# Kernel tuning notes

Measured on AMD Instinct MI355X. Metric: run time of the kernel, lower is better.

## Reference

```python
import jax, jax.numpy as jnp
import numpy as np

BETA = 0.25

def setup_inputs() -> dict:
    key = jax.random.key(0)
    kz, ke = jax.random.split(key)
    z = jax.random.normal(kz, (8, 256, 8, 32, 32), dtype=jnp.float32)
    num_codes, code_dim = 1024, 256
    # matches nn.init.uniform_(weight, -1/num_codes, 1/num_codes) in scale
    embed = jax.random.uniform(ke, (num_codes, code_dim), dtype=jnp.float32,
                               minval=-1.0 / num_codes, maxval=1.0 / num_codes)
    return {"z": z, "embed": embed}


def reference(z, embed):
    # z: (B, C, D, H, W); embed: (num_codes, code_dim) with C == code_dim
    B, C, D, H, W = z.shape
    num_codes = embed.shape[0]
    z_flat = jnp.transpose(z, (0, 2, 3, 4, 1)).reshape(-1, C)  # (N, C)

    # squared euclidean distances to all codes: ||z||^2 + ||e||^2 - 2 z.e
    dist = ((z_flat * z_flat).sum(axis=1, keepdims=True)
            + (embed * embed).sum(axis=1)
            - 2.0 * z_flat @ embed.T)  # (N, num_codes)
    indices = jnp.argmin(dist, axis=1)  # (N,) int
    z_q_flat = embed[indices]  # (N, C) gather

    # commitment loss (codebook is EMA-updated, so only beta * commitment)
    commitment = jnp.mean((z_flat - jax.lax.stop_gradient(z_q_flat)) ** 2)
    loss = BETA * commitment

    # straight-through estimator
    z_q_flat = z_flat + jax.lax.stop_gradient(z_q_flat - z_flat)
    z_q = jnp.transpose(z_q_flat.reshape(B, D, H, W, C), (0, 4, 1, 2, 3))

    # perplexity (scatter-add histogram instead of materializing one-hot)
    counts = jnp.zeros((num_codes,), dtype=z.dtype).at[indices].add(1.0)
    avg_probs = counts / indices.shape[0]
    perplexity = jnp.exp(-jnp.sum(avg_probs * jnp.log(avg_probs + 1e-10)))

    return z_q, indices.reshape(B, D, H, W), loss, perplexity
```

## Files before the change

kernel.cpp:

```cpp
#include <hip/hip_runtime.h>
#include <math.h>

#define Cdim   256
#define Ssp    8192
#define Npts   65536
#define NCODES 1024
#define BETA   0.25f
#define MT     64
#define NKC    48
#define ESCALE 8192.0f
#define WS_NEED (65536 + (size_t)786432 * 2)

typedef _Float16 f16;
typedef f16   half8  __attribute__((ext_vector_type(8)));
typedef float f32x16 __attribute__((ext_vector_type(16)));

#define MFMA16(A, B, C) __builtin_amdgcn_mfma_f32_32x32x16_f16(A, B, C, 0, 0, 0)

__global__ __launch_bounds__(256) void enorm_kernel(const float* __restrict__ embed,
                                                    float* __restrict__ enorm) {
    int j = blockIdx.x * 256 + threadIdx.x;
    if (j >= NCODES) return;
    const float4* row = reinterpret_cast<const float4*>(embed + (size_t)j * Cdim);
    float s = 0.f;
#pragma unroll 8
    for (int c4 = 0; c4 < Cdim / 4; ++c4) {
        float4 v = row[c4];
        s += v.x * v.x + v.y * v.y + v.z * v.z + v.w * v.w;
    }
    enorm[j] = s;
}

__global__ __launch_bounds__(256) void prep_kernel(const float* __restrict__ embed,
                                                   f16* __restrict__ Bws) {
    int tid = blockIdx.x * 256 + threadIdx.x;
    int o4 = tid * 4;
    int kc = o4 >> 14;
    int r  = o4 & 16383;
    int j  = r >> 4;
    int k0 = r & 15;
#pragma unroll
    for (int i = 0; i < 4; ++i) {
        int k = kc * 16 + k0 + i;
        int c = k & 255;
        float ev = embed[j * 256 + c] * ESCALE;
        f16 eh = (f16)ev;
        f16 v  = (k >= 256 && k < 512) ? (f16)(ev - (float)eh) : eh;
        Bws[o4 + i] = v;
    }
}

__global__ __launch_bounds__(256, 2) void vq_gemm(const float* __restrict__ z,
                                                  const f16* __restrict__ Bws,
                                                  const float* __restrict__ enorm,
                                                  float* __restrict__ out_idx,
                                                  float* __restrict__ counts) {
    __shared__ __attribute__((aligned(16))) f16 As[MT * 512];
    __shared__ float en_s[NCODES];
    __shared__ float znp[256];
    __shared__ float zn_s[MT];
    __shared__ float redv[8 * MT];
    __shared__ int   redi[8 * MT];

    const int t  = threadIdx.x;
    const int l  = t & 63;
    const int w  = t >> 6;
    const int ln = l & 31;
    const int kb = l >> 5;
    const int n0 = blockIdx.x * MT;
    const int b  = n0 >> 13;
    const int s0 = n0 & 8191;

    {
        const int p = t & 63;
        const int q = t >> 6;
        const float* zb = z + (size_t)b * ((size_t)Cdim * Ssp) + s0;
        float zsq = 0.f;
#pragma unroll
        for (int gi = 0; gi < 8; ++gi) {
            const int c0 = q * 64 + gi * 8;
            half8 hh, ll;
#pragma unroll
            for (int u = 0; u < 8; ++u) {
                float zv = zb[(size_t)(c0 + u) * Ssp + p];
                zsq += zv * zv;
                f16 zh = (f16)zv;
                hh[u] = zh;
                ll[u] = (f16)(zv - (float)zh);
            }
            const int g0 = c0 >> 3;
            *(half8*)&As[p * 512 + 8 * (g0 ^ (p & 7))]        = hh;
            *(half8*)&As[p * 512 + 8 * ((32 + g0) ^ (p & 7))] = ll;
        }
        znp[q * 64 + p] = zsq;
    }
    for (int i = t; i < NCODES; i += 256) en_s[i] = enorm[i];
    __syncthreads();
    if (t < MT) zn_s[t] = ((znp[t] + znp[64 + t]) + znp[128 + t]) + znp[192 + t];
    __syncthreads();

#pragma unroll 1
    for (int jh = 0; jh < 2; ++jh) {
        f32x16 acc[2][4] = {};
        const f16* bbase = Bws + (size_t)(jh * 512 + w * 128 + ln) * 16 + kb * 8;

        half8 b0 = *(const half8*)(bbase);
        half8 b1 = *(const half8*)(bbase + 512);
        half8 b2 = *(const half8*)(bbase + 1024);
        half8 b3 = *(const half8*)(bbase + 1536);

#pragma unroll 2
        for (int kc = 0; kc < NKC; ++kc) {
            const int gg = (kc < 16) ? (2 * kc + kb)
                         : (kc < 32) ? (2 * (kc - 16) + kb)
                                     : (32 + 2 * (kc - 32) + kb);
            const int gsw = 8 * (gg ^ (ln & 7));
            half8 a0 = *(const half8*)&As[ln * 512 + gsw];
            half8 a1 = *(const half8*)&As[(32 + ln) * 512 + gsw];

            half8 n0r = b0, n1 = b1, n2 = b2, n3 = b3;
            if (kc + 1 < NKC) {
                const f16* src = bbase + (size_t)(kc + 1) * 16384;
                n0r = *(const half8*)(src);
                n1  = *(const half8*)(src + 512);
                n2  = *(const half8*)(src + 1024);
                n3  = *(const half8*)(src + 1536);
            }
            acc[0][0] = MFMA16(a0, b0, acc[0][0]);
            acc[1][0] = MFMA16(a1, b0, acc[1][0]);
            acc[0][1] = MFMA16(a0, b1, acc[0][1]);
            acc[1][1] = MFMA16(a1, b1, acc[1][1]);
            acc[0][2] = MFMA16(a0, b2, acc[0][2]);
            acc[1][2] = MFMA16(a1, b2, acc[1][2]);
            acc[0][3] = MFMA16(a0, b3, acc[0][3]);
            acc[1][3] = MFMA16(a1, b3, acc[1][3]);
            b0 = n0r; b1 = n1; b2 = n2; b3 = n3;
        }

        const int h = l >> 5;
#pragma unroll
        for (int mm = 0; mm < 2; ++mm) {
#pragma unroll
            for (int rg = 0; rg < 16; ++rg) {
                const int row = mm * 32 + (rg & 3) + 8 * (rg >> 2) + 4 * h;
                const float znv = zn_s[row];
                float bv = 3.0e38f; int bi = 0;
#pragma unroll
                for (int nn = 0; nn < 4; ++nn) {
                    const int col = jh * 512 + w * 128 + nn * 32 + ln;
                    float k1 = znv + en_s[col];
                    float sc = k1 - acc[mm][nn][rg] * (2.0f / ESCALE);
                    if (sc < bv) { bv = sc; bi = col; }
                }
#pragma unroll
                for (int off = 1; off < 32; off <<= 1) {
                    float ov = __shfl_xor(bv, off, 64);
                    int   oi = __shfl_xor(bi, off, 64);
                    if (ov < bv || (ov == bv && oi < bi)) { bv = ov; bi = oi; }
                }
                if (ln == 0) {
                    redv[(jh * 4 + w) * MT + row] = bv;
                    redi[(jh * 4 + w) * MT + row] = bi;
                }
            }
        }
    }
    __syncthreads();
    if (t < MT) {
        float bv = redv[t]; int bi = redi[t];
#pragma unroll
        for (int s = 1; s < 8; ++s) {
            float ov = redv[s * MT + t]; int oi = redi[s * MT + t];
            if (ov < bv || (ov == bv && oi < bi)) { bv = ov; bi = oi; }
        }
        out_idx[n0 + t] = (float)bi;
        atomicAdd(&counts[bi], 1.0f);
    }
}

__global__ __launch_bounds__(256) void vq_epi(const float* __restrict__ z,
                                              const float* __restrict__ embed,
                                              const float* __restrict__ out_idx,
                                              float* __restrict__ out_zq,
                                              float* __restrict__ loss_acc) {
    const int n = blockIdx.x * 256 + threadIdx.x;
    const int b = n >> 13, s = n & 8191;
    const int idx = (int)out_idx[n];
    const float4* er = reinterpret_cast<const float4*>(embed + (size_t)idx * Cdim);
    const float* zp = z + (size_t)b * ((size_t)Cdim * Ssp) + s;
    float* oq = out_zq + (size_t)b * ((size_t)Cdim * Ssp) + s;
    float lsum = 0.f;
#pragma unroll 4
    for (int c4 = 0; c4 < Cdim / 4; ++c4) {
        float4 e = er[c4];
        const int c = c4 * 4;
        float z0 = zp[(size_t)(c + 0) * Ssp], z1 = zp[(size_t)(c + 1) * Ssp];
        float z2 = zp[(size_t)(c + 2) * Ssp], z3 = zp[(size_t)(c + 3) * Ssp];
        oq[(size_t)(c + 0) * Ssp] = e.x;
        oq[(size_t)(c + 1) * Ssp] = e.y;
        oq[(size_t)(c + 2) * Ssp] = e.z;
        oq[(size_t)(c + 3) * Ssp] = e.w;
        float d0 = z0 - e.x, d1 = z1 - e.y, d2 = z2 - e.z, d3 = z3 - e.w;
        lsum += d0 * d0 + d1 * d1 + d2 * d2 + d3 * d3;
    }
#pragma unroll
    for (int off = 32; off > 0; off >>= 1) lsum += __shfl_down(lsum, off, 64);
    if ((threadIdx.x & 63) == 0) atomicAdd(loss_acc, lsum);
}

#define PTS 64
#define CT  128
#define KC  32
__global__ __launch_bounds__(256, 2) void vq_main_fb(const float* __restrict__ z,
                                                     const float* __restrict__ embed,
                                                     const float* __restrict__ enorm,
                                                     float* __restrict__ out_zq,
                                                     float* __restrict__ out_idx,
                                                     float* __restrict__ loss_acc,
                                                     float* __restrict__ counts) {
    __shared__ __attribute__((aligned(16))) float smem[Cdim * PTS + KC * CT];
    float* zt = smem;
    float* et = smem + Cdim * PTS;
    const int t  = threadIdx.x;
    const int n0 = blockIdx.x * PTS;
    const int b  = n0 >> 13;
    const int s0 = n0 & 8191;
    const float* zb = z + (size_t)b * Cdim * Ssp + s0;
    {
        const int p4 = (t & 15) * 4, crow = t >> 4;
#pragma unroll
        for (int it = 0; it < 16; ++it) {
            int c = it * 16 + crow;
            float4 v = *reinterpret_cast<const float4*>(zb + (size_t)c * Ssp + p4);
            *reinterpret_cast<float4*>(&zt[c * PTS + p4]) = v;
        }
    }
    __syncthreads();
    {
        const int p = t & 63, qq = t >> 6;
        float sacc = 0.f;
#pragma unroll 8
        for (int c = qq * 64; c < qq * 64 + 64; ++c) { float v = zt[c * PTS + p]; sacc += v * v; }
        et[qq * 64 + p] = sacc;
    }
    __syncthreads();
    const int pg = t & 15, jg = t >> 4;
    const int p0 = pg * 4;
    float zn[4];
#pragma unroll
    for (int i = 0; i < 4; ++i) {
        int p = p0 + i;
        zn[i] = ((et[p] + et[64 + p]) + et[128 + p]) + et[192 + p];
    }
    float bestv[4] = {3.0e38f, 3.0e38f, 3.0e38f, 3.0e38f};
    int   besti[4] = {0, 0, 0, 0};
    const int dj = t >> 3, q = t & 7;
    const int sw_st = (q & 3) << 3;
    for (int jt = 0; jt < NCODES / CT; ++jt) {
        const int J0 = jt * CT;
        float acc[4][8];
#pragma unroll
        for (int i = 0; i < 4; ++i)
#pragma unroll
            for (int m = 0; m < 8; ++m) acc[i][m] = 0.f;
        for (int ks = 0; ks < Cdim / KC; ++ks) {
            const int cc0 = ks * KC;
            __syncthreads();
#pragma unroll
            for (int i = 0; i < 4; ++i) {
                const int jrel = dj + 32 * i;
                const float4 v = *reinterpret_cast<const float4*>(
                    embed + (size_t)(J0 + jrel) * Cdim + cc0 + q * 4);
                const int c0 = q * 4;
                const int jsw = jrel ^ sw_st;
                et[(c0 + 0) * CT + jsw] = v.x;
                et[(c0 + 1) * CT + jsw] = v.y;
                et[(c0 + 2) * CT + jsw] = v.z;
                et[(c0 + 3) * CT + jsw] = v.w;
            }
            __syncthreads();
#pragma unroll 4
            for (int c = 0; c < KC; ++c) {
                const float4 zp = *reinterpret_cast<const float4*>(&zt[(cc0 + c) * PTS + p0]);
                const int jb = (jg * 8) ^ (((c >> 2) & 3) << 3);
                const float4 ea = *reinterpret_cast<const float4*>(&et[c * CT + jb]);
                const float4 eb = *reinterpret_cast<const float4*>(&et[c * CT + jb + 4]);
                const float zc[4] = {zp.x, zp.y, zp.z, zp.w};
                const float ec[8] = {ea.x, ea.y, ea.z, ea.w, eb.x, eb.y, eb.z, eb.w};
#pragma unroll
                for (int i = 0; i < 4; ++i)
#pragma unroll
                    for (int m = 0; m < 8; ++m) acc[i][m] += zc[i] * ec[m];
            }
        }
#pragma unroll
        for (int m = 0; m < 8; ++m) {
            const int cid = J0 + jg * 8 + m;
            const float en = enorm[cid];
#pragma unroll
            for (int i = 0; i < 4; ++i) {
                float k1 = zn[i] + en;
                float sc = k1 - 2.0f * acc[i][m];
                if (sc < bestv[i]) { bestv[i] = sc; besti[i] = cid; }
            }
        }
    }
    __syncthreads();
    float* rv = et; int* ri = (int*)(et + 1024); int* idxf = (int*)(et + 2048);
#pragma unroll
    for (int i = 0; i < 4; ++i) { int p = p0 + i; rv[p * 16 + jg] = bestv[i]; ri[p * 16 + jg] = besti[i]; }
    __syncthreads();
    if (t < PTS) {
        int p = t;
        float bv = rv[p * 16]; int bi = ri[p * 16];
        for (int g = 1; g < 16; ++g) {
            float v = rv[p * 16 + g]; int ii = ri[p * 16 + g];
            if (v < bv || (v == bv && ii < bi)) { bv = v; bi = ii; }
        }
        idxf[p] = bi;
        out_idx[n0 + p] = (float)bi;
        atomicAdd(&counts[bi], 1.0f);
    }
    __syncthreads();
    float lsum = 0.f;
    {
        const int p = t & 63, cbase = t >> 6;
        const int myidx = idxf[p];
        const float4* erow4 = reinterpret_cast<const float4*>(embed + (size_t)myidx * Cdim);
        float* ob = out_zq + (size_t)b * Cdim * Ssp + s0 + p;
#pragma unroll 4
        for (int pass = 0; pass < 16; ++pass) {
            int c = cbase * 64 + pass * 4;
            float4 e = erow4[c >> 2];
            ob[(size_t)(c + 0) * Ssp] = e.x;
            ob[(size_t)(c + 1) * Ssp] = e.y;
            ob[(size_t)(c + 2) * Ssp] = e.z;
            ob[(size_t)(c + 3) * Ssp] = e.w;
            float d0 = zt[(c + 0) * PTS + p] - e.x;
            float d1 = zt[(c + 1) * PTS + p] - e.y;
            float d2 = zt[(c + 2) * PTS + p] - e.z;
            float d3 = zt[(c + 3) * PTS + p] - e.w;
            lsum += d0 * d0 + d1 * d1 + d2 * d2 + d3 * d3;
        }
    }
#pragma unroll
    for (int off = 32; off > 0; off >>= 1) lsum += __shfl_down(lsum, off, 64);
    if ((t & 63) == 0) atomicAdd(loss_acc, lsum);
}

__global__ __launch_bounds__(1024) void vq_final(const float* __restrict__ counts,
                                                 const float* __restrict__ loss_acc,
                                                 float* __restrict__ out_loss,
                                                 float* __restrict__ out_perp) {
    __shared__ float red[16];
    int t = threadIdx.x;
    float cnt = counts[t];
    float avg = cnt * (1.0f / (float)Npts);
    float term = avg * logf(avg + 1e-10f);
#pragma unroll
    for (int off = 32; off > 0; off >>= 1) term += __shfl_down(term, off, 64);
    if ((t & 63) == 0) red[t >> 6] = term;
    __syncthreads();
    if (t == 0) {
        float s = 0.f;
        for (int i = 0; i < 16; ++i) s += red[i];
        *out_perp = expf(-s);
        *out_loss = BETA * loss_acc[0] * (1.0f / 16777216.0f);
    }
}

extern "C" void kernel_launch(void* const* d_in, const int* in_sizes, int n_in,
                              void* d_out, int out_size, void* d_ws, size_t ws_size,
                              hipStream_t stream) {
    const float* z     = (const float*)d_in[0];
    const float* embed = (const float*)d_in[1];

    float* ws       = (float*)d_ws;
    float* loss_acc = ws;
    float* counts   = ws + 64;
    float* enorm    = ws + 2048;

    float* out_zq   = (float*)d_out;
    float* out_idx  = out_zq + (size_t)Npts * Cdim;
    float* out_loss = out_idx + Npts;
    float* out_perp = out_loss + 1;

    hipMemsetAsync(d_ws, 0, 2048 * sizeof(float), stream);
    enorm_kernel<<<NCODES / 256, 256, 0, stream>>>(embed, enorm);

    if (ws_size >= WS_NEED) {
        f16* Bws = (f16*)((char*)d_ws + 65536);
        prep_kernel<<<768, 256, 0, stream>>>(embed, Bws);
        vq_gemm<<<Npts / MT, 256, 0, stream>>>(z, Bws, enorm, out_idx, counts);
        vq_epi<<<Npts / 256, 256, 0, stream>>>(z, embed, out_idx, out_zq, loss_acc);
    } else {
        vq_main_fb<<<Npts / PTS, 256, 0, stream>>>(z, embed, enorm, out_zq, out_idx,
                                                   loss_acc, counts);
    }
    vq_final<<<1, 1024, 0, stream>>>(counts, loss_acc, out_loss, out_perp);
}
```

Before: 224.4 us.

## Fuse epilogue gather and loss into GEMM kernel, double-buffer B loads

Removes the separate epilogue kernel. The GEMM kernel now writes the gathered codebook rows to z_q directly with nontemporal stores. It computes the commitment loss from the winning distance value instead of re-reading z. The MFMA loop is restructured into a two-stage register double buffer for B fragments, and z reads use nontemporal loads. The fused path saves a full re-read of z and a launch. The risk is that the loss computed from the fp16-split distance may differ slightly in precision, and register pressure rises.

Measured after the change: 278.2 us. +24.0%, slower.

```diff
diff --git a/kernel.cpp b/kernel.cpp
--- a/kernel.cpp
+++ b/kernel.cpp
@@ -52,8 +52,11 @@
 
 __global__ __launch_bounds__(256, 2) void vq_gemm(const float* __restrict__ z,
                                                   const f16* __restrict__ Bws,
+                                                  const float* __restrict__ embed,
                                                   const float* __restrict__ enorm,
+                                                  float* __restrict__ out_zq,
                                                   float* __restrict__ out_idx,
+                                                  float* __restrict__ loss_acc,
                                                   float* __restrict__ counts) {
     __shared__ __attribute__((aligned(16))) f16 As[MT * 512];
     __shared__ float en_s[NCODES];
@@ -61,6 +64,7 @@
     __shared__ float zn_s[MT];
     __shared__ float redv[8 * MT];
     __shared__ int   redi[8 * MT];
+    __shared__ int   idxf[MT];
 
     const int t  = threadIdx.x;
     const int l  = t & 63;
@@ -82,7 +86,7 @@
             half8 hh, ll;
 #pragma unroll
             for (int u = 0; u < 8; ++u) {
-                float zv = zb[(size_t)(c0 + u) * Ssp + p];
+                float zv = __builtin_nontemporal_load(zb + (size_t)(c0 + u) * Ssp + p);
                 zsq += zv * zv;
                 f16 zh = (f16)zv;
                 hh[u] = zh;
@@ -104,37 +108,62 @@
         f32x16 acc[2][4] = {};
         const f16* bbase = Bws + (size_t)(jh * 512 + w * 128 + ln) * 16 + kb * 8;
 
-        half8 b0 = *(const half8*)(bbase);
-        half8 b1 = *(const half8*)(bbase + 512);
-        half8 b2 = *(const half8*)(bbase + 1024);
-        half8 b3 = *(const half8*)(bbase + 1536);
-
-#pragma unroll 2
-        for (int kc = 0; kc < NKC; ++kc) {
-            const int gg = (kc < 16) ? (2 * kc + kb)
-                         : (kc < 32) ? (2 * (kc - 16) + kb)
-                                     : (32 + 2 * (kc - 32) + kb);
-            const int gsw = 8 * (gg ^ (ln & 7));
-            half8 a0 = *(const half8*)&As[ln * 512 + gsw];
-            half8 a1 = *(const half8*)&As[(32 + ln) * 512 + gsw];
-
-            half8 n0r = b0, n1 = b1, n2 = b2, n3 = b3;
-            if (kc + 1 < NKC) {
-                const f16* src = bbase + (size_t)(kc + 1) * 16384;
-                n0r = *(const half8*)(src);
-                n1  = *(const half8*)(src + 512);
-                n2  = *(const half8*)(src + 1024);
-                n3  = *(const half8*)(src + 1536);
-            }
-            acc[0][0] = MFMA16(a0, b0, acc[0][0]);
-            acc[1][0] = MFMA16(a1, b0, acc[1][0]);
-            acc[0][1] = MFMA16(a0, b1, acc[0][1]);
-            acc[1][1] = MFMA16(a1, b1, acc[1][1]);
-            acc[0][2] = MFMA16(a0, b2, acc[0][2]);
-            acc[1][2] = MFMA16(a1, b2, acc[1][2]);
-            acc[0][3] = MFMA16(a0, b3, acc[0][3]);
-            acc[1][3] = MFMA16(a1, b3, acc[1][3]);
-            b0 = n0r; b1 = n1; b2 = n2; b3 = n3;
+        half8 bA0 = *(const half8*)(bbase);
+        half8 bA1 = *(const half8*)(bbase + 512);
+        half8 bA2 = *(const half8*)(bbase + 1024);
+        half8 bA3 = *(const half8*)(bbase + 1536);
+        const f16* s1 = bbase + 16384;
+        half8 bB0 = *(const half8*)(s1);
+        half8 bB1 = *(const half8*)(s1 + 512);
+        half8 bB2 = *(const half8*)(s1 + 1024);
+        half8 bB3 = *(const half8*)(s1 + 1536);
+
+#pragma unroll 1
+        for (int kc = 0; kc < NKC; kc += 2) {
+            const int base = (kc < 16) ? (2 * kc) : (kc < 32) ? (2 * (kc - 16))
+                                                              : (32 + 2 * (kc - 32));
+            const int ggA = base + kb;
+            const int ggB = base + 2 + kb;
+            half8 aA0 = *(const half8*)&As[ln * 512 + 8 * (ggA ^ (ln & 7))];
+            half8 aA1 = *(const half8*)&As[(32 + ln) * 512 + 8 * (ggA ^ (ln & 7))];
+            half8 aB0 = *(const half8*)&As[ln * 512 + 8 * (ggB ^ (ln & 7))];
+            half8 aB1 = *(const half8*)&As[(32 + ln) * 512 + 8 * (ggB ^ (ln & 7))];
+
+            acc[0][0] = MFMA16(aA0, bA0, acc[0][0]);
+            acc[1][0] = MFMA16(aA1, bA0, acc[1][0]);
+            acc[0][1] = MFMA16(aA0, bA1, acc[0][1]);
+            acc[1][1] = MFMA16(aA1, bA1, acc[1][1]);
+            acc[0][2] = MFMA16(aA0, bA2, acc[0][2]);
+            acc[1][2] = MFMA16(aA1, bA2, acc[1][2]);
+            acc[0][3] = MFMA16(aA0, bA3, acc[0][3]);
+            acc[1][3] = MFMA16(aA1, bA3, acc[1][3]);
+
+            {
+                const int pf = (kc + 2 < NKC) ? kc + 2 : NKC - 1;
+                const f16* src = bbase + (size_t)pf * 16384;
+                bA0 = *(const half8*)(src);
+                bA1 = *(const half8*)(src + 512);
+                bA2 = *(const half8*)(src + 1024);
+                bA3 = *(const half8*)(src + 1536);
+            }
+
+            acc[0][0] = MFMA16(aB0, bB0, acc[0][0]);
+            acc[1][0] = MFMA16(aB1, bB0, acc[1][0]);
+            acc[0][1] = MFMA16(aB0, bB1, acc[0][1]);
+            acc[1][1] = MFMA16(aB1, bB1, acc[1][1]);
+            acc[0][2] = MFMA16(aB0, bB2, acc[0][2]);
+            acc[1][2] = MFMA16(aB1, bB2, acc[1][2]);
+            acc[0][3] = MFMA16(aB0, bB3, acc[0][3]);
+            acc[1][3] = MFMA16(aB1, bB3, acc[1][3]);
+
+            {
+                const int pf = (kc + 3 < NKC) ? kc + 3 : NKC - 1;
+                const f16* src = bbase + (size_t)pf * 16384;
+                bB0 = *(const half8*)(src);
+                bB1 = *(const half8*)(src + 512);
+                bB2 = *(const half8*)(src + 1024);
+                bB3 = *(const half8*)(src + 1536);
+            }
         }
 
         const int h = l >> 5;
@@ -166,6 +195,7 @@
         }
     }
     __syncthreads();
+
     if (t < MT) {
         float bv = redv[t]; int bi = redi[t];
 #pragma unroll
@@ -174,38 +204,31 @@
             if (ov < bv || (ov == bv && oi < bi)) { bv = ov; bi = oi; }
         }
         out_idx[n0 + t] = (float)bi;
+        idxf[t] = bi;
         atomicAdd(&counts[bi], 1.0f);
-    }
-}
-
-__global__ __launch_bounds__(256) void vq_epi(const float* __restrict__ z,
-                                              const float* __restrict__ embed,
-                                              const float* __restrict__ out_idx,
-                                              float* __restrict__ out_zq,
-                                              float* __restrict__ loss_acc) {
-    const int n = blockIdx.x * 256 + threadIdx.x;
-    const int b = n >> 13, s = n & 8191;
-    const int idx = (int)out_idx[n];
-    const float4* er = reinterpret_cast<const float4*>(embed + (size_t)idx * Cdim);
-    const float* zp = z + (size_t)b * ((size_t)Cdim * Ssp) + s;
-    float* oq = out_zq + (size_t)b * ((size_t)Cdim * Ssp) + s;
-    float lsum = 0.f;
+        float lsum = bv;
+#pragma unroll
+        for (int off = 32; off > 0; off >>= 1) lsum += __shfl_down(lsum, off, 64);
+        if (t == 0) atomicAdd(loss_acc, lsum);
+    }
+    __syncthreads();
+
+    {
+        const int p     = t & 63;
+        const int cbase = t >> 6;
+        const int myidx = idxf[p];
+        const float4* erow4 = reinterpret_cast<const float4*>(embed + (size_t)myidx * Cdim);
+        float* ob = out_zq + (size_t)b * ((size_t)Cdim * Ssp) + s0 + p;
 #pragma unroll 4
-    for (int c4 = 0; c4 < Cdim / 4; ++c4) {
-        float4 e = er[c4];
-        const int c = c4 * 4;
-        float z0 = zp[(size_t)(c + 0) * Ssp], z1 = zp[(size_t)(c + 1) * Ssp];
-        float z2 = zp[(size_t)(c + 2) * Ssp], z3 = zp[(size_t)(c + 3) * Ssp];
-        oq[(size_t)(c + 0) * Ssp] = e.x;
-        oq[(size_t)(c + 1) * Ssp] = e.y;
-        oq[(size_t)(c + 2) * Ssp] = e.z;
-        oq[(size_t)(c + 3) * Ssp] = e.w;
-        float d0 = z0 - e.x, d1 = z1 - e.y, d2 = z2 - e.z, d3 = z3 - e.w;
-        lsum += d0 * d0 + d1 * d1 + d2 * d2 + d3 * d3;
-    }
-#pragma unroll
-    for (int off = 32; off > 0; off >>= 1) lsum += __shfl_down(lsum, off, 64);
-    if ((threadIdx.x & 63) == 0) atomicAdd(loss_acc, lsum);
+        for (int pass = 0; pass < 16; ++pass) {
+            int c = cbase * 64 + pass * 4;
+            float4 e = erow4[c >> 2];
+            __builtin_nontemporal_store(e.x, ob + (size_t)(c + 0) * Ssp);
+            __builtin_nontemporal_store(e.y, ob + (size_t)(c + 1) * Ssp);
+            __builtin_nontemporal_store(e.z, ob + (size_t)(c + 2) * Ssp);
+            __builtin_nontemporal_store(e.w, ob + (size_t)(c + 3) * Ssp);
+        }
+    }
 }
 
 #define PTS 64
@@ -391,8 +414,8 @@
     if (ws_size >= WS_NEED) {
         f16* Bws = (f16*)((char*)d_ws + 65536);
         prep_kernel<<<768, 256, 0, stream>>>(embed, Bws);
-        vq_gemm<<<Npts / MT, 256, 0, stream>>>(z, Bws, enorm, out_idx, counts);
-        vq_epi<<<Npts / 256, 256, 0, stream>>>(z, embed, out_idx, out_zq, loss_acc);
+        vq_gemm<<<Npts / MT, 256, 0, stream>>>(z, Bws, embed, enorm, out_zq,
+                                               out_idx, loss_acc, counts);
     } else {
         vq_main_fb<<<Npts / PTS, 256, 0, stream>>>(z, embed, enorm, out_zq, out_idx,
                                                    loss_acc, counts);
```

## Derive loss from GEMM min distances, drop z reread, deepen B prefetch

Applied to the files above, without the earlier changes.

The commitment loss is now summed from the per-point minimum distance the GEMM kernel already computes, so the epilogue no longer rereads all of z and only scatters codebook rows, using nontemporal stores. The GEMM inner loop is unrolled by six, with a three-stage rotating register prefetch of B tiles and double-buffered A fragments from shared memory, to hide global and LDS latency. Loads of z are marked nontemporal. The loss now comes from the expanded-form distance (||z||²+||e||²−2z·e, with split-fp16 products), which may differ numerically from the direct squared difference, and the extra prefetch registers may cost occupancy.

New measurement: 234.8 us. +4.6%, slower.

```diff
diff --git a/kernel.cpp b/kernel.cpp
--- a/kernel.cpp
+++ b/kernel.cpp
@@ -50,10 +50,36 @@
     }
 }
 
+#define GG(k) (((k) < 16) ? (2 * (k) + kb) : ((k) < 32) ? (2 * ((k) - 16) + kb) \
+                                                        : (32 + 2 * ((k) - 32) + kb))
+
+#define ABODY(kcv, BB, AC0, AC1, AN0, AN1)                               \
+    {                                                                    \
+        const int kcn = ((kcv) + 1 < NKC) ? (kcv) + 1 : NKC - 1;         \
+        const int ggn = GG(kcn);                                         \
+        AN0 = *(const half8*)&As[ln * 512 + 8 * (ggn ^ (ln & 7))];       \
+        AN1 = *(const half8*)&As[(32 + ln) * 512 + 8 * (ggn ^ (ln & 7))];\
+        acc[0][0] = MFMA16(AC0, BB[0], acc[0][0]);                       \
+        acc[1][0] = MFMA16(AC1, BB[0], acc[1][0]);                       \
+        acc[0][1] = MFMA16(AC0, BB[1], acc[0][1]);                       \
+        acc[1][1] = MFMA16(AC1, BB[1], acc[1][1]);                       \
+        acc[0][2] = MFMA16(AC0, BB[2], acc[0][2]);                       \
+        acc[1][2] = MFMA16(AC1, BB[2], acc[1][2]);                       \
+        acc[0][3] = MFMA16(AC0, BB[3], acc[0][3]);                       \
+        acc[1][3] = MFMA16(AC1, BB[3], acc[1][3]);                       \
+        const int pf = ((kcv) + 3 < NKC) ? (kcv) + 3 : NKC - 1;          \
+        const f16* src = bbase + (size_t)pf * 16384;                     \
+        BB[0] = *(const half8*)(src);                                    \
+        BB[1] = *(const half8*)(src + 512);                              \
+        BB[2] = *(const half8*)(src + 1024);                             \
+        BB[3] = *(const half8*)(src + 1536);                             \
+    }
+
 __global__ __launch_bounds__(256, 2) void vq_gemm(const float* __restrict__ z,
                                                   const f16* __restrict__ Bws,
                                                   const float* __restrict__ enorm,
                                                   float* __restrict__ out_idx,
+                                                  float* __restrict__ loss_acc,
                                                   float* __restrict__ counts) {
     __shared__ __attribute__((aligned(16))) f16 As[MT * 512];
     __shared__ float en_s[NCODES];
@@ -82,7 +108,7 @@
             half8 hh, ll;
 #pragma unroll
             for (int u = 0; u < 8; ++u) {
-                float zv = zb[(size_t)(c0 + u) * Ssp + p];
+                float zv = __builtin_nontemporal_load(zb + (size_t)(c0 + u) * Ssp + p);
                 zsq += zv * zv;
                 f16 zh = (f16)zv;
                 hh[u] = zh;
@@ -104,37 +130,29 @@
         f32x16 acc[2][4] = {};
         const f16* bbase = Bws + (size_t)(jh * 512 + w * 128 + ln) * 16 + kb * 8;
 
-        half8 b0 = *(const half8*)(bbase);
-        half8 b1 = *(const half8*)(bbase + 512);
-        half8 b2 = *(const half8*)(bbase + 1024);
-        half8 b3 = *(const half8*)(bbase + 1536);
-
-#pragma unroll 2
-        for (int kc = 0; kc < NKC; ++kc) {
-            const int gg = (kc < 16) ? (2 * kc + kb)
-                         : (kc < 32) ? (2 * (kc - 16) + kb)
-                                     : (32 + 2 * (kc - 32) + kb);
-            const int gsw = 8 * (gg ^ (ln & 7));
-            half8 a0 = *(const half8*)&As[ln * 512 + gsw];
-            half8 a1 = *(const half8*)&As[(32 + ln) * 512 + gsw];
-
-            half8 n0r = b0, n1 = b1, n2 = b2, n3 = b3;
-            if (kc + 1 < NKC) {
-                const f16* src = bbase + (size_t)(kc + 1) * 16384;
-                n0r = *(const half8*)(src);
-                n1  = *(const half8*)(src + 512);
-                n2  = *(const half8*)(src + 1024);
-                n3  = *(const half8*)(src + 1536);
-            }
-            acc[0][0] = MFMA16(a0, b0, acc[0][0]);
-            acc[1][0] = MFMA16(a1, b0, acc[1][0]);
-            acc[0][1] = MFMA16(a0, b1, acc[0][1]);
-            acc[1][1] = MFMA16(a1, b1, acc[1][1]);
-            acc[0][2] = MFMA16(a0, b2, acc[0][2]);
-            acc[1][2] = MFMA16(a1, b2, acc[1][2]);
-            acc[0][3] = MFMA16(a0, b3, acc[0][3]);
-            acc[1][3] = MFMA16(a1, b3, acc[1][3]);
-            b0 = n0r; b1 = n1; b2 = n2; b3 = n3;
+        half8 b0[4], b1[4], b2[4];
+#pragma unroll
+        for (int i = 0; i < 4; ++i) b0[i] = *(const half8*)(bbase + i * 512);
+#pragma unroll
+        for (int i = 0; i < 4; ++i) b1[i] = *(const half8*)(bbase + 16384 + i * 512);
+#pragma unroll
+        for (int i = 0; i < 4; ++i) b2[i] = *(const half8*)(bbase + 32768 + i * 512);
+
+        half8 aC0, aC1, aD0, aD1;
+        {
+            const int gg0 = GG(0);
+            aC0 = *(const half8*)&As[ln * 512 + 8 * (gg0 ^ (ln & 7))];
+            aC1 = *(const half8*)&As[(32 + ln) * 512 + 8 * (gg0 ^ (ln & 7))];
+        }
+
+#pragma unroll 1
+        for (int kc = 0; kc < NKC; kc += 6) {
+            ABODY(kc + 0, b0, aC0, aC1, aD0, aD1)
+            ABODY(kc + 1, b1, aD0, aD1, aC0, aC1)
+            ABODY(kc + 2, b2, aC0, aC1, aD0, aD1)
+            ABODY(kc + 3, b0, aD0, aD1, aC0, aC1)
+            ABODY(kc + 4, b1, aC0, aC1, aD0, aD1)
+            ABODY(kc + 5, b2, aD0, aD1, aC0, aC1)
         }
 
         const int h = l >> 5;
@@ -166,6 +184,7 @@
         }
     }
     __syncthreads();
+
     if (t < MT) {
         float bv = redv[t]; int bi = redi[t];
 #pragma unroll
@@ -175,37 +194,30 @@
         }
         out_idx[n0 + t] = (float)bi;
         atomicAdd(&counts[bi], 1.0f);
-    }
-}
-
-__global__ __launch_bounds__(256) void vq_epi(const float* __restrict__ z,
-                                              const float* __restrict__ embed,
+        float lsum = bv;
+#pragma unroll
+        for (int off = 32; off > 0; off >>= 1) lsum += __shfl_down(lsum, off, 64);
+        if (t == 0) atomicAdd(loss_acc, lsum);
+    }
+}
+
+__global__ __launch_bounds__(256) void vq_epi(const float* __restrict__ embed,
                                               const float* __restrict__ out_idx,
-                                              float* __restrict__ out_zq,
-                                              float* __restrict__ loss_acc) {
+                                              float* __restrict__ out_zq) {
     const int n = blockIdx.x * 256 + threadIdx.x;
     const int b = n >> 13, s = n & 8191;
     const int idx = (int)out_idx[n];
     const float4* er = reinterpret_cast<const float4*>(embed + (size_t)idx * Cdim);
-    const float* zp = z + (size_t)b * ((size_t)Cdim * Ssp) + s;
     float* oq = out_zq + (size_t)b * ((size_t)Cdim * Ssp) + s;
-    float lsum = 0.f;
 #pragma unroll 4
     for (int c4 = 0; c4 < Cdim / 4; ++c4) {
         float4 e = er[c4];
         const int c = c4 * 4;
-        float z0 = zp[(size_t)(c + 0) * Ssp], z1 = zp[(size_t)(c + 1) * Ssp];
-        float z2 = zp[(size_t)(c + 2) * Ssp], z3 = zp[(size_t)(c + 3) * Ssp];
-        oq[(size_t)(c + 0) * Ssp] = e.x;
-        oq[(size_t)(c + 1) * Ssp] = e.y;
-        oq[(size_t)(c + 2) * Ssp] = e.z;
-        oq[(size_t)(c + 3) * Ssp] = e.w;
-        float d0 = z0 - e.x, d1 = z1 - e.y, d2 = z2 - e.z, d3 = z3 - e.w;
-        lsum += d0 * d0 + d1 * d1 + d2 * d2 + d3 * d3;
-    }
-#pragma unroll
-    for (int off = 32; off > 0; off >>= 1) lsum += __shfl_down(lsum, off, 64);
-    if ((threadIdx.x & 63) == 0) atomicAdd(loss_acc, lsum);
+        __builtin_nontemporal_store(e.x, oq + (size_t)(c + 0) * Ssp);
+        __builtin_nontemporal_store(e.y, oq + (size_t)(c + 1) * Ssp);
+        __builtin_nontemporal_store(e.z, oq + (size_t)(c + 2) * Ssp);
+        __builtin_nontemporal_store(e.w, oq + (size_t)(c + 3) * Ssp);
+    }
 }
 
 #define PTS 64
@@ -391,8 +403,9 @@
     if (ws_size >= WS_NEED) {
         f16* Bws = (f16*)((char*)d_ws + 65536);
         prep_kernel<<<768, 256, 0, stream>>>(embed, Bws);
-        vq_gemm<<<Npts / MT, 256, 0, stream>>>(z, Bws, enorm, out_idx, counts);
-        vq_epi<<<Npts / 256, 256, 0, stream>>>(z, embed, out_idx, out_zq, loss_acc);
+        vq_gemm<<<Npts / MT, 256, 0, stream>>>(z, Bws, enorm, out_idx,
+                                               loss_acc, counts);
+        vq_epi<<<Npts / 256, 256, 0, stream>>>(embed, out_idx, out_zq);
     } else {
         vq_main_fb<<<Npts / PTS, 256, 0, stream>>>(z, embed, enorm, out_zq, out_idx,
                                                    loss_acc, counts);
```

## Double GEMM tile to 128 points with 8 waves and fold loss into argmin

Applied to the files above, without the earlier changes.

The GEMM block now covers 128 points with 512 threads arranged as 2 row-waves by 4 column-waves, so each B fragment loaded from global memory serves twice as many rows. The commitment loss is taken from the minimum distance value computed in the GEMM epilogue, so the epilogue kernel no longer re-reads z and only writes z_q, using nontemporal stores. LDS use roughly doubles (As is now 128 KB), which may limit occupancy to one block per CU despite the launch bound of 2. The loss now comes from the expanded-form distance, which can differ slightly from the direct squared difference.

Result: faster. 207.8 us (-7.4%).

```diff
diff --git a/kernel.cpp b/kernel.cpp
--- a/kernel.cpp
+++ b/kernel.cpp
@@ -6,7 +6,7 @@
 #define Npts   65536
 #define NCODES 1024
 #define BETA   0.25f
-#define MT     64
+#define MT     128
 #define NKC    48
 #define ESCALE 8192.0f
 #define WS_NEED (65536 + (size_t)786432 * 2)
@@ -50,14 +50,18 @@
     }
 }
 
-__global__ __launch_bounds__(256, 2) void vq_gemm(const float* __restrict__ z,
+#define GG(k) (((k) < 16) ? (2 * (k) + kb) : ((k) < 32) ? (2 * ((k) - 16) + kb) \
+                                                        : (32 + 2 * ((k) - 32) + kb))
+
+__global__ __launch_bounds__(512, 2) void vq_gemm(const float* __restrict__ z,
                                                   const f16* __restrict__ Bws,
                                                   const float* __restrict__ enorm,
                                                   float* __restrict__ out_idx,
+                                                  float* __restrict__ loss_acc,
                                                   float* __restrict__ counts) {
     __shared__ __attribute__((aligned(16))) f16 As[MT * 512];
     __shared__ float en_s[NCODES];
-    __shared__ float znp[256];
+    __shared__ float znp[4 * MT];
     __shared__ float zn_s[MT];
     __shared__ float redv[8 * MT];
     __shared__ int   redi[8 * MT];
@@ -65,6 +69,8 @@
     const int t  = threadIdx.x;
     const int l  = t & 63;
     const int w  = t >> 6;
+    const int wm = w >> 2;
+    const int wn = w & 3;
     const int ln = l & 31;
     const int kb = l >> 5;
     const int n0 = blockIdx.x * MT;
@@ -72,8 +78,8 @@
     const int s0 = n0 & 8191;
 
     {
-        const int p = t & 63;
-        const int q = t >> 6;
+        const int p = t & 127;
+        const int q = t >> 7;
         const float* zb = z + (size_t)b * ((size_t)Cdim * Ssp) + s0;
         float zsq = 0.f;
 #pragma unroll
@@ -92,31 +98,31 @@
             *(half8*)&As[p * 512 + 8 * (g0 ^ (p & 7))]        = hh;
             *(half8*)&As[p * 512 + 8 * ((32 + g0) ^ (p & 7))] = ll;
         }
-        znp[q * 64 + p] = zsq;
-    }
-    for (int i = t; i < NCODES; i += 256) en_s[i] = enorm[i];
-    __syncthreads();
-    if (t < MT) zn_s[t] = ((znp[t] + znp[64 + t]) + znp[128 + t]) + znp[192 + t];
+        znp[q * MT + p] = zsq;
+    }
+    for (int i = t; i < NCODES; i += 512) en_s[i] = enorm[i];
+    __syncthreads();
+    if (t < MT)
+        zn_s[t] = ((znp[t] + znp[MT + t]) + znp[2 * MT + t]) + znp[3 * MT + t];
     __syncthreads();
 
 #pragma unroll 1
     for (int jh = 0; jh < 2; ++jh) {
         f32x16 acc[2][4] = {};
-        const f16* bbase = Bws + (size_t)(jh * 512 + w * 128 + ln) * 16 + kb * 8;
+        const f16* bbase = Bws + (size_t)(jh * 512 + wn * 128 + ln) * 16 + kb * 8;
 
         half8 b0 = *(const half8*)(bbase);
         half8 b1 = *(const half8*)(bbase + 512);
         half8 b2 = *(const half8*)(bbase + 1024);
         half8 b3 = *(const half8*)(bbase + 1536);
 
+        const int rowA = wm * 64 + ln;
 #pragma unroll 2
         for (int kc = 0; kc < NKC; ++kc) {
-            const int gg = (kc < 16) ? (2 * kc + kb)
-                         : (kc < 32) ? (2 * (kc - 16) + kb)
-                                     : (32 + 2 * (kc - 32) + kb);
+            const int gg  = GG(kc);
             const int gsw = 8 * (gg ^ (ln & 7));
-            half8 a0 = *(const half8*)&As[ln * 512 + gsw];
-            half8 a1 = *(const half8*)&As[(32 + ln) * 512 + gsw];
+            half8 a0 = *(const half8*)&As[rowA * 512 + gsw];
+            half8 a1 = *(const half8*)&As[(rowA + 32) * 512 + gsw];
 
             half8 n0r = b0, n1 = b1, n2 = b2, n3 = b3;
             if (kc + 1 < NKC) {
@@ -142,12 +148,12 @@
         for (int mm = 0; mm < 2; ++mm) {
 #pragma unroll
             for (int rg = 0; rg < 16; ++rg) {
-                const int row = mm * 32 + (rg & 3) + 8 * (rg >> 2) + 4 * h;
+                const int row = wm * 64 + mm * 32 + (rg & 3) + 8 * (rg >> 2) + 4 * h;
                 const float znv = zn_s[row];
                 float bv = 3.0e38f; int bi = 0;
 #pragma unroll
                 for (int nn = 0; nn < 4; ++nn) {
-                    const int col = jh * 512 + w * 128 + nn * 32 + ln;
+                    const int col = jh * 512 + wn * 128 + nn * 32 + ln;
                     float k1 = znv + en_s[col];
                     float sc = k1 - acc[mm][nn][rg] * (2.0f / ESCALE);
                     if (sc < bv) { bv = sc; bi = col; }
@@ -159,13 +165,14 @@
                     if (ov < bv || (ov == bv && oi < bi)) { bv = ov; bi = oi; }
                 }
                 if (ln == 0) {
-                    redv[(jh * 4 + w) * MT + row] = bv;
-                    redi[(jh * 4 + w) * MT + row] = bi;
+                    redv[(jh * 4 + wn) * MT + row] = bv;
+                    redi[(jh * 4 + wn) * MT + row] = bi;
                 }
             }
         }
     }
     __syncthreads();
+
     if (t < MT) {
         float bv = redv[t]; int bi = redi[t];
 #pragma unroll
@@ -175,37 +182,30 @@
         }
         out_idx[n0 + t] = (float)bi;
         atomicAdd(&counts[bi], 1.0f);
-    }
-}
-
-__global__ __launch_bounds__(256) void vq_epi(const float* __restrict__ z,
-                                              const float* __restrict__ embed,
+        float lsum = bv;
+#pragma unroll
+        for (int off = 32; off > 0; off >>= 1) lsum += __shfl_down(lsum, off, 64);
+        if ((t & 63) == 0) atomicAdd(loss_acc, lsum);
+    }
+}
+
+__global__ __launch_bounds__(256) void vq_epi(const float* __restrict__ embed,
                                               const float* __restrict__ out_idx,
-                                              float* __restrict__ out_zq,
-                                              float* __restrict__ loss_acc) {
+                                              float* __restrict__ out_zq) {
     const int n = blockIdx.x * 256 + threadIdx.x;
     const int b = n >> 13, s = n & 8191;
     const int idx = (int)out_idx[n];
     const float4* er = reinterpret_cast<const float4*>(embed + (size_t)idx * Cdim);
-    const float* zp = z + (size_t)b * ((size_t)Cdim * Ssp) + s;
     float* oq = out_zq + (size_t)b * ((size_t)Cdim * Ssp) + s;
-    float lsum = 0.f;
 #pragma unroll 4
     for (int c4 = 0; c4 < Cdim / 4; ++c4) {
         float4 e = er[c4];
         const int c = c4 * 4;
-        float z0 = zp[(size_t)(c + 0) * Ssp], z1 = zp[(size_t)(c + 1) * Ssp];
-        float z2 = zp[(size_t)(c + 2) * Ssp], z3 = zp[(size_t)(c + 3) * Ssp];
-        oq[(size_t)(c + 0) * Ssp] = e.x;
-        oq[(size_t)(c + 1) * Ssp] = e.y;
-        oq[(size_t)(c + 2) * Ssp] = e.z;
-        oq[(size_t)(c + 3) * Ssp] = e.w;
-        float d0 = z0 - e.x, d1 = z1 - e.y, d2 = z2 - e.z, d3 = z3 - e.w;
-        lsum += d0 * d0 + d1 * d1 + d2 * d2 + d3 * d3;
-    }
-#pragma unroll
-    for (int off = 32; off > 0; off >>= 1) lsum += __shfl_down(lsum, off, 64);
-    if ((threadIdx.x & 63) == 0) atomicAdd(loss_acc, lsum);
+        __builtin_nontemporal_store(e.x, oq + (size_t)(c + 0) * Ssp);
+        __builtin_nontemporal_store(e.y, oq + (size_t)(c + 1) * Ssp);
+        __builtin_nontemporal_store(e.z, oq + (size_t)(c + 2) * Ssp);
+        __builtin_nontemporal_store(e.w, oq + (size_t)(c + 3) * Ssp);
+    }
 }
 
 #define PTS 64
@@ -391,8 +391,9 @@
     if (ws_size >= WS_NEED) {
         f16* Bws = (f16*)((char*)d_ws + 65536);
         prep_kernel<<<768, 256, 0, stream>>>(embed, Bws);
-        vq_gemm<<<Npts / MT, 256, 0, stream>>>(z, Bws, enorm, out_idx, counts);
-        vq_epi<<<Npts / 256, 256, 0, stream>>>(z, embed, out_idx, out_zq, loss_acc);
+        vq_gemm<<<Npts / MT, 512, 0, stream>>>(z, Bws, enorm, out_idx,
+                                               loss_acc, counts);
+        vq_epi<<<Npts / 256, 256, 0, stream>>>(embed, out_idx, out_zq);
     } else {
         vq_main_fb<<<Npts / PTS, 256, 0, stream>>>(z, embed, enorm, out_zq, out_idx,
                                                    loss_acc, counts);
```
